# Kernel optimization log

Measured on AMD Instinct MI355X. Metric: run time of the kernel, lower is better.

Reference implementation:

```python
import jax, jax.numpy as jnp
import numpy as np

B, C, S = 4, 512, 8192   # batch, channels, seq len
E = 256                  # q_dim // r1 = projected dim
D = 256                  # dilaion: block size; window width = 2*D (D even)


def setup_inputs() -> dict:
    key = jax.random.key(0)
    ks = jax.random.split(key, 6)
    w = 0.05
    return {
        "x1": jax.random.normal(ks[0], (B, C, S), jnp.float32),
        "mask": jnp.ones((B, 1, S), jnp.float32),
        "Wq": jax.random.normal(ks[1], (E, C), jnp.float32) * w,
        "bq": jnp.zeros((E,), jnp.float32),
        "Wk": jax.random.normal(ks[2], (E, C), jnp.float32) * w,
        "bk": jnp.zeros((E,), jnp.float32),
        "Wv": jax.random.normal(ks[3], (E, C), jnp.float32) * w,
        "bv": jnp.zeros((E,), jnp.float32),
        "Wo": jax.random.normal(ks[4], (C, E), jnp.float32) * w,
        "bo": jnp.zeros((C,), jnp.float32),
    }


def _windows(x, nb, d):
    # x: [B, ch, S] -> nb overlapping windows of width 2d (stride d, halo d//2 each side)
    b, ch, _ = x.shape
    xp = jnp.pad(x, ((0, 0), (0, 0), (d // 2, d // 2)))  # [B, ch, S + d]
    lo = xp[:, :, : nb * d].reshape(b, ch, nb, d)
    hi = xp[:, :, d:].reshape(b, ch, nb, d)
    return jnp.concatenate([lo, hi], axis=-1).transpose(0, 2, 1, 3)  # [B, nb, ch, 2d]


def reference(x1, mask, Wq, bq, Wk, bk, Wv, bv, Wo, bo):
    nb = S // D  # S divisible by D -> no tail padding branch
    # 1x1 conv projections
    q = jnp.einsum('ec,bcs->bes', Wq, x1) + bq[None, :, None]
    k = jnp.einsum('ec,bcs->bes', Wk, x1) + bk[None, :, None]
    v = jnp.einsum('ec,bcs->bes', Wv, x1) + bv[None, :, None]

    qw = q.reshape(B, E, nb, D).transpose(0, 2, 1, 3)   # [B, nb, E, D]
    kw = _windows(k, nb, D)                              # [B, nb, E, 2D]
    vw = _windows(v, nb, D)                              # [B, nb, E, 2D]
    pm = mask[:, 0:1, :]                                 # padding mask [B,1,S]
    pmw = _windows(pm, nb, D)                            # [B, nb, 1, 2D]

    W = 2 * D
    # original loop `window_mask[:, :, i:i+D] = 1 for i in range(D)` -> union covers
    # columns [0, 2D-2]; only the last column stays 0 (rows identical)
    win = (jnp.arange(W) < W - 1).astype(jnp.float32)    # [2D]
    fmask = win[None, None, None, :] * pmw               # [B, nb, 1, 2D]

    energy = jnp.einsum('bneq,bnek->bnqk', qw, kw) / np.float32(np.sqrt(E))
    attn = jax.nn.softmax(energy + jnp.log(fmask + 1e-6), axis=-1) * fmask
    out = jnp.einsum('bnek,bnqk->bneq', vw, attn)        # [B, nb, E, D]

    h = jax.nn.gelu(out, approximate=False)
    h = jnp.einsum('oe,bneq->bnoq', Wo, h) + bo[None, None, :, None]  # [B, nb, C, D]
    y = h.transpose(0, 2, 1, 3).reshape(B, C, nb * D)[:, :, :S]
    return y * mask[:, 0:1, :]
```

## Files before the change

### kernel.cpp

```cpp
#include <hip/hip_runtime.h>
#include <hip/hip_bf16.h>

typedef __attribute__((ext_vector_type(8))) short short8;
typedef __attribute__((ext_vector_type(4))) float f32x4;
typedef __attribute__((ext_vector_type(4))) int int4v;

#define DI __device__ __forceinline__

constexpr int Bq = 4, Cc = 512, Ss = 8192, Ee = 256;
constexpr int SP = 8448;
constexpr long XSLAB = 4194304;

DI unsigned short f2bf(float f) {
    unsigned int u = __float_as_uint(f);
    unsigned int r = u + 0x7fffu + ((u >> 16) & 1u);
    return (unsigned short)(r >> 16);
}

union U16x8 { int4v v; unsigned short u[8]; };

DI void gll16(const void* g, void* l) {
    __builtin_amdgcn_global_load_lds(
        (const __attribute__((address_space(1))) unsigned int*)g,
        (__attribute__((address_space(3))) unsigned int*)l, 16, 0, 0);
}

DI unsigned pkbf(float lo, float hi) {
    unsigned r;
    asm("v_cvt_pk_bf16_f32 %0, %1, %2" : "=v"(r) : "v"(lo), "v"(hi));
    return r;
}

DI short8 mk8(unsigned a, unsigned b, unsigned c, unsigned d) {
    int4v v; v[0] = (int)a; v[1] = (int)b; v[2] = (int)c; v[3] = (int)d;
    union { int4v i; short8 s; } U; U.i = v; return U.s;
}

DI f32x4 max4(f32x4 a, f32x4 b) {
    f32x4 r;
    r[0] = fmaxf(a[0], b[0]); r[1] = fmaxf(a[1], b[1]);
    r[2] = fmaxf(a[2], b[2]); r[3] = fmaxf(a[3], b[3]);
    return r;
}

DI float gelu_t(float x) {
    float x2 = x * x;
    float z = x * (0.7978845608f + 0.0356774081f * x2);
    float az = fabsf(z);
    float e = __expf(-2.f * az);
    float th = (1.f - e) / (1.f + e);
    th = (z < 0.f) ? -th : th;
    return 0.5f * x * (1.f + th);
}

DI int SIG(int k)  { return ((k & 4) << 2) | ((k & 24) >> 1) | (k & 3); }
DI int SIG2(int k) { return SIG(SIG(k)); }

__global__ __launch_bounds__(256) void kprep(
    const float* __restrict__ Wq, const float* __restrict__ Wk, const float* __restrict__ Wv,
    const float* __restrict__ Wo, unsigned short* __restrict__ Wqkv_b, unsigned short* __restrict__ Wo_b,
    unsigned short* __restrict__ kTp, unsigned short* __restrict__ vp)
{
    int blk = blockIdx.x, t = threadIdx.x;
    if (blk < 1536) {
        int i = blk * 256 + t;
        if (i < 768 * 512) {
            int m = i >> 9, c = i & 511;
            const float* src = (m < 256) ? Wq : ((m < 512) ? Wk : Wv);
            Wqkv_b[i] = f2bf(src[(m & 255) * 512 + c]);
        }
        if (i < 512 * 256) {
            int kap = i & 255;
            int src = (i & ~255) | (kap & ~31) | SIG(kap & 31);
            Wo_b[i] = f2bf(Wo[src]);
        }
    } else {
        int i = (blk - 1536) * 256 + t;
        int4v z = {0, 0, 0, 0};
        if (i < 32768) {
            int b = i >> 13, r = i & 8191;
            int side = r >> 12, off = r & 4095;
            *(int4v*)(kTp + (long)b * SP * 256 + (long)(side ? 8320 : 0) * 256 + off * 8) = z;
        } else {
            int j = i - 32768;
            int b = j >> 13, r = j & 8191;
            int row = r >> 5, side = (r >> 4) & 1, sc = r & 15;
            *(int4v*)(vp + ((long)b * 256 + row) * SP + side * 8320 + sc * 8) = z;
        }
    }
}

__global__ __launch_bounds__(256) void ktr_x(const float* __restrict__ x1g, unsigned short* __restrict__ xT4)
{
    const float* x1b = x1g + (long)blockIdx.y * Cc * Ss;
    unsigned short* xT = xT4 + (long)blockIdx.y * XSLAB;
    __shared__ unsigned short tile[64][72];
    int t = threadIdx.x;
    int bs = blockIdx.x & 127, bc = blockIdx.x >> 7;
    int s0 = bs * 64, c0 = bc * 64;
    int cl = t >> 4, sl = (t & 15) * 4;
    for (int it = 0; it < 4; ++it) {
        int c = cl + it * 16;
        float4 vv = *(const float4*)(x1b + (long)(c0 + c) * Ss + s0 + sl);
        tile[c][sl + 0] = f2bf(vv.x);
        tile[c][sl + 1] = f2bf(vv.y);
        tile[c][sl + 2] = f2bf(vv.z);
        tile[c][sl + 3] = f2bf(vv.w);
    }
    __syncthreads();
    int s_loc = t >> 2, cseg = (t & 3) * 16;
    for (int half = 0; half < 2; ++half) {
        U16x8 u;
        for (int j = 0; j < 8; ++j) u.u[j] = tile[cseg + half * 8 + j][s_loc];
        *(int4v*)(xT + (long)(s0 + s_loc) * Cc + c0 + cseg + half * 8) = u.v;
    }
}

__global__ __launch_bounds__(256) void kqkv(
    const unsigned short* __restrict__ xT4, const unsigned short* __restrict__ Wqkv,
    const float* __restrict__ bq, const float* __restrict__ bk, const float* __restrict__ bv,
    unsigned short* __restrict__ qT, unsigned short* __restrict__ kTp, unsigned short* __restrict__ vp,
    int b0)
{
    __shared__ int4v As[1024], Bs[1024];
    int b = b0 + blockIdx.y;
    const unsigned short* xT = xT4 + (long)blockIdx.y * XSLAB;
    int wg = blockIdx.x;
    int type = wg >> 7, id = wg & 127;
    const unsigned short *A, *Bt; unsigned short* Op;
    long opitch; const float* bias; bool biasRow;
    if (type < 2) {
        int mt = id >> 1, nt = id & 1;
        A  = xT + (long)(mt * 128) * 512;
        Bt = Wqkv + (long)(type * 256 + nt * 128) * 512;
        if (type == 0)
            Op = qT + (long)b * Ss * Ee + (long)(mt * 128) * Ee + nt * 128;
        else
            Op = kTp + (long)b * SP * Ee + (long)(128 + mt * 128) * Ee + nt * 128;
        opitch = Ee;
        bias = (type ? bk : bq) + nt * 128;
        biasRow = false;
    } else {
        int mt = id >> 6, nt = id & 63;
        A  = Wqkv + (long)(512 + mt * 128) * 512;
        Bt = xT + (long)(nt * 128) * 512;
        Op = vp + (long)b * Ee * SP + (long)(mt * 128) * SP + 128 + nt * 128;
        opitch = SP;
        bias = bv + mt * 128;
        biasRow = true;
    }
    int t = threadIdx.x, lane = t & 63, wv = t >> 6;
    int wr = (wv >> 1) * 64, wc = (wv & 1) * 64;

    int soff[4];
    #pragma unroll
    for (int i = 0; i < 4; ++i) {
        int seg = t + 256 * i, row = seg >> 3, cs = seg & 7;
        soff[i] = row * 512 + ((cs ^ (row & 7)) * 8);
    }
    char* adst = (char*)As + wv * 1024;
    char* bdst = (char*)Bs + wv * 1024;

    f32x4 acc[4][4] = {};
    for (int kk = 0; kk < 8; ++kk) {
        #pragma unroll
        for (int i = 0; i < 4; ++i) {
            gll16(A  + soff[i] + kk * 64, adst + i * 4096);
            gll16(Bt + soff[i] + kk * 64, bdst + i * 4096);
        }
        asm volatile("s_waitcnt vmcnt(0)" ::: "memory");
        __syncthreads();
        for (int ks = 0; ks < 2; ++ks) {
            int csk = ks * 4 + (lane >> 4);
            short8 af[4], bfr[4];
            #pragma unroll
            for (int mi = 0; mi < 4; ++mi) {
                int m = wr + mi * 16 + (lane & 15);
                af[mi] = *(const short8*)&As[m * 8 + (csk ^ (m & 7))];
            }
            #pragma unroll
            for (int ni = 0; ni < 4; ++ni) {
                int nn = wc + ni * 16 + (lane & 15);
                bfr[ni] = *(const short8*)&Bs[nn * 8 + (csk ^ (nn & 7))];
            }
            #pragma unroll
            for (int mi = 0; mi < 4; ++mi)
                #pragma unroll
                for (int ni = 0; ni < 4; ++ni)
                    acc[mi][ni] = __builtin_amdgcn_mfma_f32_16x16x32_bf16(af[mi], bfr[ni], acc[mi][ni], 0, 0, 0);
        }
        __syncthreads();
    }
    for (int mi = 0; mi < 4; ++mi)
        for (int ni = 0; ni < 4; ++ni) {
            int mrow = wr + mi * 16 + ((lane >> 4) * 4);
            int ncol = wc + ni * 16 + (lane & 15);
            int nc2 = biasRow ? ((ncol & ~31) | SIG2(ncol & 31)) : ncol;
            for (int r = 0; r < 4; ++r) {
                float bval = biasRow ? bias[mrow + r] : bias[ncol];
                Op[(long)(mrow + r) * opitch + nc2] = f2bf(acc[mi][ni][r] + bval);
            }
        }
}

__global__ __launch_bounds__(256, 2) void kattn(
    const unsigned short* __restrict__ qT, const unsigned short* __restrict__ kTp,
    const unsigned short* __restrict__ vp,  const unsigned short* __restrict__ Wo_b,
    const float* __restrict__ mask, const float* __restrict__ bo,
    float* __restrict__ y)
{
    __shared__ __align__(16) char SH[71680];
    float* fmaskL  = (float*)(SH + 65536);
    float* l2maskL = (float*)(SH + 67584);
    float* boL     = (float*)(SH + 69632);

    int t = threadIdx.x, lane = t & 63, wv = t >> 6;
    int G = lane >> 4, l15 = lane & 15;

    int phys = blockIdx.x;
    int L = (phys & 7) * 64 + (phys >> 3);
    int qq = L & 3, n = (L >> 2) & 31, b = L >> 7;
    int sqw = n * 256 + qq * 64 + wv * 16;

    short8 qfrag[8];
    #pragma unroll
    for (int s = 0; s < 8; ++s)
        qfrag[s] = *(const short8*)(qT + ((long)b * Ss + sqw + l15) * 256 + 32 * s + 8 * G);

    for (int i = t; i < 512; i += 256) {
        int sw = n * 256 - 128 + i;
        float f = 0.f;
        if (i != 511 && sw >= 0 && sw < Ss) f = mask[(long)b * Ss + sw];
        fmaskL[i] = f;
        l2maskL[i] = __log2f(f + 1e-6f);
    }
    if (t < 128) ((float4*)boL)[t] = ((const float4*)bo)[t];

    const unsigned short* ksrcp[4];
    const unsigned short* vsrcp[4];
    #pragma unroll
    for (int i = 0; i < 4; ++i) {
        int krow = wv * 8 + i * 2 + (lane >> 5);
        ksrcp[i] = kTp + ((long)b * SP + n * 256 + krow) * 256 + (((lane & 31) ^ (krow & 7)) * 8);
        int erow = wv * 64 + i * 16 + (lane >> 2);
        vsrcp[i] = vp + ((long)b * 256 + erow) * SP + n * 256 + (((lane & 3) ^ ((lane >> 2) & 3)) * 8);
    }

#define STAGE(CH, BUF) {                                                      \
        char* kl = SH + (BUF) * 16384 + wv * 4096;                            \
        char* vl = SH + 32768 + (BUF) * 16384 + wv * 4096;                    \
        _Pragma("unroll")                                                     \
        for (int i = 0; i < 4; ++i) gll16(ksrcp[i] + (long)(CH) * 8192, kl + i * 1024); \
        _Pragma("unroll")                                                     \
        for (int i = 0; i < 4; ++i) gll16(vsrcp[i] + (CH) * 32, vl + i * 1024);          \
    }

    STAGE(0, 0)
    STAGE(1, 1)
    asm volatile("s_waitcnt vmcnt(4) lgkmcnt(0)" ::: "memory");
    __builtin_amdgcn_s_barrier();

    float mrun = -1e30f, lrun = 0.f;
    f32x4 oacc[16] = {};

    #pragma unroll 2
    for (int ch = 0; ch < 16; ++ch) {
        const char* KB = SH + (ch & 1) * 16384;
        const char* VB = SH + 32768 + (ch & 1) * 16384;

        f32x4 eacc[2] = {};
        __builtin_amdgcn_s_setprio(1);
        #pragma unroll
        for (int s = 0; s < 8; ++s) {
            short8 kf[2];
            #pragma unroll
            for (int tt = 0; tt < 2; ++tt)
                kf[tt] = *(const short8*)(KB + (16 * tt + l15) * 512 + (((4 * s + G) ^ (l15 & 7)) * 16));
            #pragma unroll
            for (int tt = 0; tt < 2; ++tt)
                eacc[tt] = __builtin_amdgcn_mfma_f32_16x16x32_bf16(kf[tt], qfrag[s], eacc[tt], 0, 0, 0);
        }
        __builtin_amdgcn_s_setprio(0);

        int w0 = ch * 32;
        f32x4 lm[2], fm[2];
        #pragma unroll
        for (int tt = 0; tt < 2; ++tt) {
            lm[tt] = *(const f32x4*)&l2maskL[w0 + 16 * tt + 4 * G];
            fm[tt] = *(const f32x4*)&fmaskL[w0 + 16 * tt + 4 * G];
        }

        f32x4 ev[2];
        #pragma unroll
        for (int tt = 0; tt < 2; ++tt)
            ev[tt] = eacc[tt] * 0.09016844f + lm[tt];
        f32x4 m4 = max4(ev[0], ev[1]);
        float cm = fmaxf(fmaxf(m4[0], m4[1]), fmaxf(m4[2], m4[3]));
        cm = fmaxf(cm, __shfl_xor(cm, 16));
        cm = fmaxf(cm, __shfl_xor(cm, 32));
        if (__any(cm > mrun + 11.5416f)) {
            float mn = fmaxf(mrun, cm);
            float sc = exp2f(mrun - mn);
            mrun = mn; lrun *= sc;
            #pragma unroll
            for (int et = 0; et < 16; ++et) oacc[et] *= sc;
        }

        unsigned pc[4];
        float ssum = 0.f;
        #pragma unroll
        for (int tt = 0; tt < 2; ++tt) {
            f32x4 p;
            p[0] = exp2f(ev[tt][0] - mrun);
            p[1] = exp2f(ev[tt][1] - mrun);
            p[2] = exp2f(ev[tt][2] - mrun);
            p[3] = exp2f(ev[tt][3] - mrun);
            ssum += (p[0] + p[1]) + (p[2] + p[3]);
            f32x4 pf = p * fm[tt];
            pc[2 * tt]     = pkbf(pf[0], pf[1]);
            pc[2 * tt + 1] = pkbf(pf[2], pf[3]);
        }
        ssum += __shfl_xor(ssum, 16);
        ssum += __shfl_xor(ssum, 32);
        lrun += ssum;

        __builtin_amdgcn_s_setprio(1);
        {
            short8 pf = mk8(pc[0], pc[1], pc[2], pc[3]);
            #pragma unroll
            for (int et = 0; et < 16; ++et) {
                short8 vf = *(const short8*)(VB + (16 * et + l15) * 64 + ((G ^ (l15 & 3)) * 16));
                oacc[et] = __builtin_amdgcn_mfma_f32_16x16x32_bf16(vf, pf, oacc[et], 0, 0, 0);
            }
        }
        __builtin_amdgcn_s_setprio(0);

        asm volatile("s_waitcnt lgkmcnt(0)" ::: "memory");
        __builtin_amdgcn_s_barrier();
        if (ch < 14) {
            STAGE(ch + 2, ch & 1)
            asm volatile("s_waitcnt vmcnt(4)" ::: "memory");
        } else if (ch == 14) {
            asm volatile("s_waitcnt vmcnt(0)" ::: "memory");
        }
        __builtin_amdgcn_s_barrier();
    }

    float linv = 1.f / lrun;
    unsigned hc[32];
    #pragma unroll
    for (int et = 0; et < 16; ++et) {
        f32x4 xv = oacc[et] * linv;
        hc[2 * et]     = pkbf(gelu_t(xv[0]), gelu_t(xv[1]));
        hc[2 * et + 1] = pkbf(gelu_t(xv[2]), gelu_t(xv[3]));
    }
    float ym = fmaskL[128 + qq * 64 + wv * 16 + l15];

    const unsigned short* wsrcp[4];
    #pragma unroll
    for (int i = 0; i < 4; ++i) {
        int wrow = wv * 8 + i * 2 + (lane >> 5);
        wsrcp[i] = Wo_b + (long)wrow * 256 + (((lane & 31) ^ (wrow & 7)) * 8);
    }
#define WSTAGE(ST, BUF) {                                                     \
        char* wl = SH + (BUF) * 16384 + wv * 4096;                            \
        _Pragma("unroll")                                                     \
        for (int i = 0; i < 4; ++i) gll16(wsrcp[i] + (ST) * 8192, wl + i * 1024); \
    }

    WSTAGE(0, 0)
    WSTAGE(1, 1)
    asm volatile("s_waitcnt vmcnt(4)" ::: "memory");
    __builtin_amdgcn_s_barrier();

    #pragma unroll 2
    for (int step = 0; step < 16; ++step) {
        const char* WB = SH + (step & 1) * 16384;
        __builtin_amdgcn_s_setprio(1);
        #pragma unroll
        for (int otl = 0; otl < 2; ++otl) {
            f32x4 pacc = {};
            #pragma unroll
            for (int s = 0; s < 8; ++s) {
                short8 wf = *(const short8*)(WB + (16 * otl + l15) * 512 + (((4 * s + G) ^ (l15 & 7)) * 16));
                short8 hs = mk8(hc[4 * s], hc[4 * s + 1], hc[4 * s + 2], hc[4 * s + 3]);
                pacc = __builtin_amdgcn_mfma_f32_16x16x32_bf16(wf, hs, pacc, 0, 0, 0);
            }
            int o0 = step * 32 + 16 * otl + 4 * G;
            f32x4 bo4 = *(const f32x4*)&boL[o0];
            #pragma unroll
            for (int r = 0; r < 4; ++r)
                y[((long)b * Cc + o0 + r) * Ss + sqw + l15] = (pacc[r] + bo4[r]) * ym;
        }
        __builtin_amdgcn_s_setprio(0);
        asm volatile("s_waitcnt lgkmcnt(0)" ::: "memory");
        __builtin_amdgcn_s_barrier();
        if (step < 14) {
            WSTAGE(step + 2, step & 1)
            asm volatile("s_waitcnt vmcnt(4)" ::: "memory");
        } else if (step == 14) {
            asm volatile("s_waitcnt vmcnt(0)" ::: "memory");
        }
        __builtin_amdgcn_s_barrier();
    }
#undef STAGE
#undef WSTAGE
}

extern "C" void kernel_launch(void* const* d_in, const int* in_sizes, int n_in,
                              void* d_out, int out_size, void* d_ws, size_t ws_size,
                              hipStream_t stream)
{
    const float* x1   = (const float*)d_in[0];
    const float* mask = (const float*)d_in[1];
    const float* Wq   = (const float*)d_in[2];
    const float* bq   = (const float*)d_in[3];
    const float* Wk   = (const float*)d_in[4];
    const float* bk   = (const float*)d_in[5];
    const float* Wv   = (const float*)d_in[6];
    const float* bv   = (const float*)d_in[7];
    const float* Wo   = (const float*)d_in[8];
    const float* bo   = (const float*)d_in[9];
    float* y = (float*)d_out;

    if (ws_size < 60817408u) return;
    char* w = (char*)d_ws;
    unsigned short* Wqkv_b = (unsigned short*)(w);
    unsigned short* Wo_b   = (unsigned short*)(w + 786432);
    unsigned short* qT     = (unsigned short*)(w + 1048576);
    unsigned short* kTp    = (unsigned short*)(w + 17825792);
    unsigned short* vp     = (unsigned short*)(w + 35127296);
    unsigned short* xT4    = (unsigned short*)(w + 52428800);

    int g = (int)((ws_size - 52428800u) / 8388608u);
    if (g < 1) g = 1;
    if (g > 4) g = 4;

    kprep<<<1792, 256, 0, stream>>>(Wq, Wk, Wv, Wo, Wqkv_b, Wo_b, kTp, vp);
    for (int b0 = 0; b0 < 4; b0 += g) {
        int gy = (4 - b0 < g) ? (4 - b0) : g;
        ktr_x<<<dim3(1024, gy), 256, 0, stream>>>(x1 + (long)b0 * Cc * Ss, xT4);
        kqkv<<<dim3(384, gy), 256, 0, stream>>>(xT4, Wqkv_b, bq, bk, bv, qT, kTp, vp, b0);
    }
    kattn<<<512, 256, 0, stream>>>(qT, kTp, vp, Wo_b, mask, bo, y);
}
```

Measured before the change: 123.6 us.

## Fuse x transpose into prep kernel, reuse output buffer, widen attention blocks

Merges the x1 transpose/bf16 conversion into the weight-prep kernel and stores the transposed activations in the output buffer instead of workspace. This lets all batches run in a single QKV launch and removes the per-batch launch loop. The attention kernel moves to 512-thread blocks covering 128 query rows each, halving per-wave staging loads. It also issues the first Wo stage early, during the last attention chunk. Reusing the output buffer as scratch relies on kattn fully overwriting it. The larger blocks change occupancy and LDS sharing.

After: 171.5 us. +38.7%, slower.

```diff
diff --git a/kernel.cpp b/kernel.cpp
--- a/kernel.cpp
+++ b/kernel.cpp
@@ -56,14 +56,39 @@
 DI int SIG(int k)  { return ((k & 4) << 2) | ((k & 24) >> 1) | (k & 3); }
 DI int SIG2(int k) { return SIG(SIG(k)); }
 
-__global__ __launch_bounds__(256) void kprep(
+__global__ __launch_bounds__(256) void kpre(
+    const float* __restrict__ x1,
     const float* __restrict__ Wq, const float* __restrict__ Wk, const float* __restrict__ Wv,
     const float* __restrict__ Wo, unsigned short* __restrict__ Wqkv_b, unsigned short* __restrict__ Wo_b,
-    unsigned short* __restrict__ kTp, unsigned short* __restrict__ vp)
+    unsigned short* __restrict__ kTp, unsigned short* __restrict__ vp,
+    unsigned short* __restrict__ xTo)
 {
     int blk = blockIdx.x, t = threadIdx.x;
-    if (blk < 1536) {
-        int i = blk * 256 + t;
+    if (blk < 4096) {
+        int bb = blk >> 10, inner = blk & 1023;
+        const float* x1b = x1 + (long)bb * Cc * Ss;
+        unsigned short* xT = xTo + (long)bb * XSLAB;
+        __shared__ unsigned short tile[64][72];
+        int bs = inner & 127, bc = inner >> 7;
+        int s0 = bs * 64, c0 = bc * 64;
+        int cl = t >> 4, sl = (t & 15) * 4;
+        for (int it = 0; it < 4; ++it) {
+            int c = cl + it * 16;
+            float4 vv = *(const float4*)(x1b + (long)(c0 + c) * Ss + s0 + sl);
+            tile[c][sl + 0] = f2bf(vv.x);
+            tile[c][sl + 1] = f2bf(vv.y);
+            tile[c][sl + 2] = f2bf(vv.z);
+            tile[c][sl + 3] = f2bf(vv.w);
+        }
+        __syncthreads();
+        int s_loc = t >> 2, cseg = (t & 3) * 16;
+        for (int half = 0; half < 2; ++half) {
+            U16x8 u;
+            for (int j = 0; j < 8; ++j) u.u[j] = tile[cseg + half * 8 + j][s_loc];
+            *(int4v*)(xT + (long)(s0 + s_loc) * Cc + c0 + cseg + half * 8) = u.v;
+        }
+    } else if (blk < 5632) {
+        int i = (blk - 4096) * 256 + t;
         if (i < 768 * 512) {
             int m = i >> 9, c = i & 511;
             const float* src = (m < 256) ? Wq : ((m < 512) ? Wk : Wv);
@@ -75,7 +100,7 @@
             Wo_b[i] = f2bf(Wo[src]);
         }
     } else {
-        int i = (blk - 1536) * 256 + t;
+        int i = (blk - 5632) * 256 + t;
         int4v z = {0, 0, 0, 0};
         if (i < 32768) {
             int b = i >> 13, r = i & 8191;
@@ -90,41 +115,14 @@
     }
 }
 
-__global__ __launch_bounds__(256) void ktr_x(const float* __restrict__ x1g, unsigned short* __restrict__ xT4)
-{
-    const float* x1b = x1g + (long)blockIdx.y * Cc * Ss;
-    unsigned short* xT = xT4 + (long)blockIdx.y * XSLAB;
-    __shared__ unsigned short tile[64][72];
-    int t = threadIdx.x;
-    int bs = blockIdx.x & 127, bc = blockIdx.x >> 7;
-    int s0 = bs * 64, c0 = bc * 64;
-    int cl = t >> 4, sl = (t & 15) * 4;
-    for (int it = 0; it < 4; ++it) {
-        int c = cl + it * 16;
-        float4 vv = *(const float4*)(x1b + (long)(c0 + c) * Ss + s0 + sl);
-        tile[c][sl + 0] = f2bf(vv.x);
-        tile[c][sl + 1] = f2bf(vv.y);
-        tile[c][sl + 2] = f2bf(vv.z);
-        tile[c][sl + 3] = f2bf(vv.w);
-    }
-    __syncthreads();
-    int s_loc = t >> 2, cseg = (t & 3) * 16;
-    for (int half = 0; half < 2; ++half) {
-        U16x8 u;
-        for (int j = 0; j < 8; ++j) u.u[j] = tile[cseg + half * 8 + j][s_loc];
-        *(int4v*)(xT + (long)(s0 + s_loc) * Cc + c0 + cseg + half * 8) = u.v;
-    }
-}
-
 __global__ __launch_bounds__(256) void kqkv(
     const unsigned short* __restrict__ xT4, const unsigned short* __restrict__ Wqkv,
     const float* __restrict__ bq, const float* __restrict__ bk, const float* __restrict__ bv,
-    unsigned short* __restrict__ qT, unsigned short* __restrict__ kTp, unsigned short* __restrict__ vp,
-    int b0)
+    unsigned short* __restrict__ qT, unsigned short* __restrict__ kTp, unsigned short* __restrict__ vp)
 {
     __shared__ int4v As[1024], Bs[1024];
-    int b = b0 + blockIdx.y;
-    const unsigned short* xT = xT4 + (long)blockIdx.y * XSLAB;
+    int b = blockIdx.y;
+    const unsigned short* xT = xT4 + (long)b * XSLAB;
     int wg = blockIdx.x;
     int type = wg >> 7, id = wg & 127;
     const unsigned short *A, *Bt; unsigned short* Op;
@@ -203,7 +201,7 @@
         }
 }
 
-__global__ __launch_bounds__(256, 2) void kattn(
+__global__ __launch_bounds__(512, 4) void kattn(
     const unsigned short* __restrict__ qT, const unsigned short* __restrict__ kTp,
     const unsigned short* __restrict__ vp,  const unsigned short* __restrict__ Wo_b,
     const float* __restrict__ mask, const float* __restrict__ bo,
@@ -218,16 +216,18 @@
     int G = lane >> 4, l15 = lane & 15;
 
     int phys = blockIdx.x;
-    int L = (phys & 7) * 64 + (phys >> 3);
-    int qq = L & 3, n = (L >> 2) & 31, b = L >> 7;
-    int sqw = n * 256 + qq * 64 + wv * 16;
+    int xx = phys & 7, kk2 = phys >> 3;
+    int L = ((xx + 8 * (kk2 >> 1)) << 1) | (kk2 & 1);
+    int qh = L & 1, n = (L >> 1) & 31, b = L >> 6;
+    int sqw = n * 256 + qh * 128 + wv * 16;
 
     short8 qfrag[8];
     #pragma unroll
     for (int s = 0; s < 8; ++s)
         qfrag[s] = *(const short8*)(qT + ((long)b * Ss + sqw + l15) * 256 + 32 * s + 8 * G);
 
-    for (int i = t; i < 512; i += 256) {
+    {
+        int i = t;
         int sw = n * 256 - 128 + i;
         float f = 0.f;
         if (i != 511 && sw >= 0 && sw < Ss) f = mask[(long)b * Ss + sw];
@@ -236,23 +236,31 @@
     }
     if (t < 128) ((float4*)boL)[t] = ((const float4*)bo)[t];
 
-    const unsigned short* ksrcp[4];
-    const unsigned short* vsrcp[4];
+    const unsigned short* ksrcp[2];
+    const unsigned short* vsrcp[2];
+    const unsigned short* wsrcp[2];
     #pragma unroll
-    for (int i = 0; i < 4; ++i) {
-        int krow = wv * 8 + i * 2 + (lane >> 5);
+    for (int i = 0; i < 2; ++i) {
+        int krow = wv * 4 + i * 2 + (lane >> 5);
         ksrcp[i] = kTp + ((long)b * SP + n * 256 + krow) * 256 + (((lane & 31) ^ (krow & 7)) * 8);
-        int erow = wv * 64 + i * 16 + (lane >> 2);
+        int erow = wv * 32 + i * 16 + (lane >> 2);
         vsrcp[i] = vp + ((long)b * 256 + erow) * SP + n * 256 + (((lane & 3) ^ ((lane >> 2) & 3)) * 8);
+        int wrow = wv * 4 + i * 2 + (lane >> 5);
+        wsrcp[i] = Wo_b + (long)wrow * 256 + (((lane & 31) ^ (wrow & 7)) * 8);
     }
 
 #define STAGE(CH, BUF) {                                                      \
-        char* kl = SH + (BUF) * 16384 + wv * 4096;                            \
-        char* vl = SH + 32768 + (BUF) * 16384 + wv * 4096;                    \
+        char* kl = SH + (BUF) * 16384 + wv * 2048;                            \
+        char* vl = SH + 32768 + (BUF) * 16384 + wv * 2048;                    \
         _Pragma("unroll")                                                     \
-        for (int i = 0; i < 4; ++i) gll16(ksrcp[i] + (long)(CH) * 8192, kl + i * 1024); \
+        for (int i = 0; i < 2; ++i) gll16(ksrcp[i] + (long)(CH) * 8192, kl + i * 1024); \
         _Pragma("unroll")                                                     \
-        for (int i = 0; i < 4; ++i) gll16(vsrcp[i] + (CH) * 32, vl + i * 1024);          \
+        for (int i = 0; i < 2; ++i) gll16(vsrcp[i] + (CH) * 32, vl + i * 1024);          \
+    }
+#define WSTAGE(ST, BUF) {                                                     \
+        char* wl = SH + (BUF) * 16384 + wv * 2048;                            \
+        _Pragma("unroll")                                                     \
+        for (int i = 0; i < 2; ++i) gll16(wsrcp[i] + (ST) * 8192, wl + i * 1024); \
     }
 
     STAGE(0, 0)
@@ -341,7 +349,8 @@
             STAGE(ch + 2, ch & 1)
             asm volatile("s_waitcnt vmcnt(4)" ::: "memory");
         } else if (ch == 14) {
-            asm volatile("s_waitcnt vmcnt(0)" ::: "memory");
+            WSTAGE(0, 0)
+            asm volatile("s_waitcnt vmcnt(2)" ::: "memory");
         }
         __builtin_amdgcn_s_barrier();
     }
@@ -354,23 +363,10 @@
         hc[2 * et]     = pkbf(gelu_t(xv[0]), gelu_t(xv[1]));
         hc[2 * et + 1] = pkbf(gelu_t(xv[2]), gelu_t(xv[3]));
     }
-    float ym = fmaskL[128 + qq * 64 + wv * 16 + l15];
-
-    const unsigned short* wsrcp[4];
-    #pragma unroll
-    for (int i = 0; i < 4; ++i) {
-        int wrow = wv * 8 + i * 2 + (lane >> 5);
-        wsrcp[i] = Wo_b + (long)wrow * 256 + (((lane & 31) ^ (wrow & 7)) * 8);
-    }
-#define WSTAGE(ST, BUF) {                                                     \
-        char* wl = SH + (BUF) * 16384 + wv * 4096;                            \
-        _Pragma("unroll")                                                     \
-        for (int i = 0; i < 4; ++i) gll16(wsrcp[i] + (ST) * 8192, wl + i * 1024); \
-    }
-
-    WSTAGE(0, 0)
+    float ym = fmaskL[128 + qh * 128 + wv * 16 + l15];
+
     WSTAGE(1, 1)
-    asm volatile("s_waitcnt vmcnt(4)" ::: "memory");
+    asm volatile("s_waitcnt vmcnt(2)" ::: "memory");
     __builtin_amdgcn_s_barrier();
 
     #pragma unroll 2
@@ -397,7 +393,7 @@
         __builtin_amdgcn_s_barrier();
         if (step < 14) {
             WSTAGE(step + 2, step & 1)
-            asm volatile("s_waitcnt vmcnt(4)" ::: "memory");
+            asm volatile("s_waitcnt vmcnt(2)" ::: "memory");
         } else if (step == 14) {
             asm volatile("s_waitcnt vmcnt(0)" ::: "memory");
         }
@@ -423,24 +419,16 @@
     const float* bo   = (const float*)d_in[9];
     float* y = (float*)d_out;
 
-    if (ws_size < 60817408u) return;
+    if (ws_size < 52428800u) return;
     char* w = (char*)d_ws;
     unsigned short* Wqkv_b = (unsigned short*)(w);
     unsigned short* Wo_b   = (unsigned short*)(w + 786432);
     unsigned short* qT     = (unsigned short*)(w + 1048576);
     unsigned short* kTp    = (unsigned short*)(w + 17825792);
     unsigned short* vp     = (unsigned short*)(w + 35127296);
-    unsigned short* xT4    = (unsigned short*)(w + 52428800);
-
-    int g = (int)((ws_size - 52428800u) / 8388608u);
-    if (g < 1) g = 1;
-    if (g > 4) g = 4;
-
-    kprep<<<1792, 256, 0, stream>>>(Wq, Wk, Wv, Wo, Wqkv_b, Wo_b, kTp, vp);
-    for (int b0 = 0; b0 < 4; b0 += g) {
-        int gy = (4 - b0 < g) ? (4 - b0) : g;
-        ktr_x<<<dim3(1024, gy), 256, 0, stream>>>(x1 + (long)b0 * Cc * Ss, xT4);
-        kqkv<<<dim3(384, gy), 256, 0, stream>>>(xT4, Wqkv_b, bq, bk, bv, qT, kTp, vp, b0);
-    }
-    kattn<<<512, 256, 0, stream>>>(qT, kTp, vp, Wo_b, mask, bo, y);
-}
+    unsigned short* xT4    = (unsigned short*)d_out;
+
+    kpre<<<5888, 256, 0, stream>>>(x1, Wq, Wk, Wv, Wo, Wqkv_b, Wo_b, kTp, vp, xT4);
+    kqkv<<<dim3(384, 4), 256, 0, stream>>>(xT4, Wqkv_b, bq, bk, bv, qT, kTp, vp);
+    kattn<<<256, 512, 0, stream>>>(qT, kTp, vp, Wo_b, mask, bo, y);
+}
```
